# Kernel tuning notes

Hardware: AMD Instinct MI355X
Metric: run time of the kernel (lower is better)

Reference implementation:

```python
import jax, jax.numpy as jnp
import numpy as np

B, NV, NC, K = 2048, 1000, 4260, 3      # formulas, vars, clauses, literals/clause
NODES = 2 * NV + NC + 1                  # per-sample: pos lits | neg lits | clauses | root
N = B * NODES
C = B * NC


def setup_inputs() -> dict:
    key = jax.random.key(0)
    k1, k2 = jax.random.split(key)
    base = jnp.arange(B, dtype=jnp.int32) * NODES
    # positive / negative literal node ids (neg literal i is nv positions after pos literal i)
    pos_idx = (base[:, None] + jnp.arange(NV, dtype=jnp.int32)).ravel()
    neg_idx = pos_idx + NV
    # each clause picks K random literals from its own sample's 2*NV literal nodes
    lits = jax.random.randint(k1, (B, NC, K), 0, 2 * NV, dtype=jnp.int32)
    or_src = (lits + base[:, None, None]).ravel()              # [E] literal node per OR edge
    or_seg = jnp.repeat(jnp.arange(C, dtype=jnp.int32), K)     # [E] clause id per OR edge
    and_seg = jnp.repeat(jnp.arange(B, dtype=jnp.int32), NC)   # [C] root id per clause
    emb = jax.random.uniform(k2, (N,), dtype=jnp.float32)      # soft assignments in [0,1]
    return {"emb": emb, "pos_idx": pos_idx, "neg_idx": neg_idx,
            "or_src": or_src, "or_seg": or_seg, "and_seg": and_seg,
            "n_clauses": C, "n_roots": B, "epoch": 10}


def reference(emb, pos_idx, neg_idx, or_src, or_seg, and_seg, n_clauses, n_roots, epoch):
    t = jnp.asarray(epoch, jnp.float32) ** (-1.2)  # annealing temperature
    # literal transform: temporary[ind==1] = 1 - emb[ind==0]
    lit = emb.at[neg_idx].set(1.0 - emb[pos_idx])
    # --- OR gates: temperature-scaled soft-max over each clause's literals ---
    v = lit[or_src]                                            # [E] gathered literal values
    m = jax.ops.segment_max(v, or_seg, num_segments=n_clauses)
    w = jnp.exp((v - m[or_seg]) / t)                           # stabilized exp weights
    num = jax.ops.segment_sum(v * w, or_seg, num_segments=n_clauses)
    den = jax.ops.segment_sum(w, or_seg, num_segments=n_clauses)
    clause = num / den                                         # [C] soft-OR per clause
    # --- AND gate: temperature-scaled soft-min over each sample's clauses ---
    mn = jax.ops.segment_min(clause, and_seg, num_segments=n_roots)
    w2 = jnp.exp(-(clause - mn[and_seg]) / t)
    num2 = jax.ops.segment_sum(clause * w2, and_seg, num_segments=n_roots)
    den2 = jax.ops.segment_sum(w2, and_seg, num_segments=n_roots)
    return num2 / den2                                         # [B] soft-SAT per sample
```

## Files before the change

kernel.cpp:

```cpp
#include <hip/hip_runtime.h>

#define TPB 256


__device__ __forceinline__ float softor3(float a, float b, float c, float invt) {
    float m  = fmaxf(fmaxf(a, b), c);
    float wa = __expf((a - m) * invt);
    float wb = __expf((b - m) * invt);
    float wc = __expf((c - m) * invt);
    return fmaf(a, wa, fmaf(b, wb, c * wc)) / (wa + wb + wc);
}

__global__ __launch_bounds__(TPB, 8) void soft_sat_kernel(
    const float* __restrict__ emb,
    const int*   __restrict__ or_src,
    const int*   __restrict__ epoch_p,
    float* __restrict__ out,
    int NV, int NC, int NODES)
{
    extern __shared__ float smem[];
    float* lit = smem;
    float* red = smem + 2 * NV;

    const int b     = blockIdx.x;
    const int tid   = threadIdx.x;
    const int lane  = tid & 63;
    const int wid   = tid >> 6;
    const int baseI = b * NODES;

    const float invt = powf((float)epoch_p[0], 1.2f);

    const float* embb = emb + baseI;
    for (int i = tid; i < NV; i += TPB) {
        float e = embb[i];
        lit[i]      = e;
        lit[i + NV] = 1.0f - e;
    }
    __syncthreads();

    const int* osb = or_src + (long long)b * NC * 3;

    float mn = 3.4e38f, n2 = 0.0f, d2 = 0.0f;

    int c0 = 0;
    for (; c0 + TPB * 4 <= NC; c0 += TPB * 4) {
        const int4* p = (const int4*)(osb + (c0 + tid * 4) * 3);
        int4 A = p[0], Bv = p[1], Cv = p[2];

        float cv0 = softor3(lit[A.x  - baseI], lit[A.y  - baseI], lit[A.z  - baseI], invt);
        float cv1 = softor3(lit[A.w  - baseI], lit[Bv.x - baseI], lit[Bv.y - baseI], invt);
        float cv2 = softor3(lit[Bv.z - baseI], lit[Bv.w - baseI], lit[Cv.x - baseI], invt);
        float cv3 = softor3(lit[Cv.y - baseI], lit[Cv.z - baseI], lit[Cv.w - baseI], invt);

        float cmin = fminf(fminf(cv0, cv1), fminf(cv2, cv3));
        float m = fminf(mn, cmin);
        float f = __expf((m - mn) * invt);
        n2 *= f; d2 *= f; mn = m;

        float w0 = __expf((mn - cv0) * invt);
        float w1 = __expf((mn - cv1) * invt);
        float w2 = __expf((mn - cv2) * invt);
        float w3 = __expf((mn - cv3) * invt);
        n2 = fmaf(cv0, w0, fmaf(cv1, w1, fmaf(cv2, w2, fmaf(cv3, w3, n2))));
        d2 += w0 + w1 + w2 + w3;
    }

    for (int c = c0 + tid; c < NC; c += TPB) {
        const int* q = osb + c * 3;
        float cv = softor3(lit[q[0] - baseI], lit[q[1] - baseI], lit[q[2] - baseI], invt);
        float m = fminf(mn, cv);
        float f = __expf((m - mn) * invt);
        n2 *= f; d2 *= f; mn = m;
        float w = __expf((mn - cv) * invt);
        n2 = fmaf(cv, w, n2);
        d2 += w;
    }

    for (int off = 32; off; off >>= 1) {
        float mo = __shfl_xor(mn, off);
        float no = __shfl_xor(n2, off);
        float dd = __shfl_xor(d2, off);
        float m  = fminf(mn, mo);
        float f1 = __expf((m - mn) * invt);
        float f2 = __expf((m - mo) * invt);
        n2 = n2 * f1 + no * f2;
        d2 = d2 * f1 + dd * f2;
        mn = m;
    }
    if (lane == 0) { red[wid * 3] = mn; red[wid * 3 + 1] = n2; red[wid * 3 + 2] = d2; }
    __syncthreads();

    if (tid == 0) {
        float M = red[0], N2 = red[1], D2 = red[2];
        for (int w = 1; w < TPB / 64; ++w) {
            float mo = red[w * 3], no = red[w * 3 + 1], dd = red[w * 3 + 2];
            float m  = fminf(M, mo);
            float f1 = __expf((m - M) * invt);
            float f2 = __expf((m - mo) * invt);
            N2 = N2 * f1 + no * f2;
            D2 = D2 * f1 + dd * f2;
            M = m;
        }
        out[b] = N2 / D2;
    }
}

extern "C" void kernel_launch(void* const* d_in, const int* in_sizes, int n_in,
                              void* d_out, int out_size, void* d_ws, size_t ws_size,
                              hipStream_t stream)
{
    const float* emb     = (const float*)d_in[0];
    const int*   or_src  = (const int*)d_in[3];
    const int*   epoch_p = (const int*)d_in[8];
    float*       out     = (float*)d_out;

    const int B     = out_size;
    const int NV    = in_sizes[1] / B;
    const int NODES = in_sizes[0] / B;
    const int C     = in_sizes[5];
    const int NC    = C / B;

    const size_t smem = (size_t)(2 * NV + 12) * sizeof(float);
    soft_sat_kernel<<<B, TPB, smem, stream>>>(emb, or_src, epoch_p, out,
                                              NV, NC, NODES);
}
```

Before: 250.2 us.

## Prefetch clause indices ahead of LDS fill and double-buffer 8 clauses per thread

Loads each thread's clause literal indices before the shared-memory literal fill, and software-pipelines the next chunk's index loads while the current chunk is being evaluated. Each thread now handles 8 clauses per iteration instead of 4. Launch bounds are relaxed to 4 blocks per SM to make room for the extra registers. The goal is to hide global-load latency on the index stream, at the cost of higher register pressure and possibly lower occupancy.

Result: no change. 251.5 us (+0.5%).

```diff
diff --git a/kernel.cpp b/kernel.cpp
--- a/kernel.cpp
+++ b/kernel.cpp
@@ -11,7 +11,9 @@
     return fmaf(a, wa, fmaf(b, wb, c * wc)) / (wa + wb + wc);
 }
 
-__global__ __launch_bounds__(TPB, 8) void soft_sat_kernel(
+#define CL(v0, v1, v2) softor3(lit[(v0) - baseI], lit[(v1) - baseI], lit[(v2) - baseI], invt)
+
+__global__ __launch_bounds__(TPB, 4) void soft_sat_kernel(
     const float* __restrict__ emb,
     const int*   __restrict__ or_src,
     const int*   __restrict__ epoch_p,
@@ -30,6 +32,15 @@
 
     const float invt = powf((float)epoch_p[0], 1.2f);
 
+    const int* osb  = or_src + (long long)b * NC * 3;
+    const int nfull = (NC / (TPB * 8)) * (TPB * 8);
+
+    int4 a0, a1, a2, a3, a4, a5;
+    if (nfull) {
+        const int4* p = (const int4*)(osb + tid * 24);
+        a0 = p[0]; a1 = p[1]; a2 = p[2]; a3 = p[3]; a4 = p[4]; a5 = p[5];
+    }
+
     const float* embb = emb + baseI;
     for (int i = tid; i < NV; i += TPB) {
         float e = embb[i];
@@ -38,21 +49,27 @@
     }
     __syncthreads();
 
-    const int* osb = or_src + (long long)b * NC * 3;
-
     float mn = 3.4e38f, n2 = 0.0f, d2 = 0.0f;
 
-    int c0 = 0;
-    for (; c0 + TPB * 4 <= NC; c0 += TPB * 4) {
-        const int4* p = (const int4*)(osb + (c0 + tid * 4) * 3);
-        int4 A = p[0], Bv = p[1], Cv = p[2];
+    for (int c0 = 0; c0 < nfull; c0 += TPB * 8) {
+        int4 b0, b1, b2, b3, b4, b5;
+        const int cn = c0 + TPB * 8;
+        if (cn < nfull) {
+            const int4* p = (const int4*)(osb + (cn + tid * 8) * 3);
+            b0 = p[0]; b1 = p[1]; b2 = p[2]; b3 = p[3]; b4 = p[4]; b5 = p[5];
+        }
 
-        float cv0 = softor3(lit[A.x  - baseI], lit[A.y  - baseI], lit[A.z  - baseI], invt);
-        float cv1 = softor3(lit[A.w  - baseI], lit[Bv.x - baseI], lit[Bv.y - baseI], invt);
-        float cv2 = softor3(lit[Bv.z - baseI], lit[Bv.w - baseI], lit[Cv.x - baseI], invt);
-        float cv3 = softor3(lit[Cv.y - baseI], lit[Cv.z - baseI], lit[Cv.w - baseI], invt);
+        float cv0 = CL(a0.x, a0.y, a0.z);
+        float cv1 = CL(a0.w, a1.x, a1.y);
+        float cv2 = CL(a1.z, a1.w, a2.x);
+        float cv3 = CL(a2.y, a2.z, a2.w);
+        float cv4 = CL(a3.x, a3.y, a3.z);
+        float cv5 = CL(a3.w, a4.x, a4.y);
+        float cv6 = CL(a4.z, a4.w, a5.x);
+        float cv7 = CL(a5.y, a5.z, a5.w);
 
-        float cmin = fminf(fminf(cv0, cv1), fminf(cv2, cv3));
+        float cmin = fminf(fminf(fminf(cv0, cv1), fminf(cv2, cv3)),
+                           fminf(fminf(cv4, cv5), fminf(cv6, cv7)));
         float m = fminf(mn, cmin);
         float f = __expf((m - mn) * invt);
         n2 *= f; d2 *= f; mn = m;
@@ -61,13 +78,20 @@
         float w1 = __expf((mn - cv1) * invt);
         float w2 = __expf((mn - cv2) * invt);
         float w3 = __expf((mn - cv3) * invt);
+        float w4 = __expf((mn - cv4) * invt);
+        float w5 = __expf((mn - cv5) * invt);
+        float w6 = __expf((mn - cv6) * invt);
+        float w7 = __expf((mn - cv7) * invt);
         n2 = fmaf(cv0, w0, fmaf(cv1, w1, fmaf(cv2, w2, fmaf(cv3, w3, n2))));
-        d2 += w0 + w1 + w2 + w3;
+        n2 = fmaf(cv4, w4, fmaf(cv5, w5, fmaf(cv6, w6, fmaf(cv7, w7, n2))));
+        d2 += (w0 + w1 + w2 + w3) + (w4 + w5 + w6 + w7);
+
+        if (cn < nfull) { a0 = b0; a1 = b1; a2 = b2; a3 = b3; a4 = b4; a5 = b5; }
     }
 
-    for (int c = c0 + tid; c < NC; c += TPB) {
+    for (int c = nfull + tid; c < NC; c += TPB) {
         const int* q = osb + c * 3;
-        float cv = softor3(lit[q[0] - baseI], lit[q[1] - baseI], lit[q[2] - baseI], invt);
+        float cv = CL(q[0], q[1], q[2]);
         float m = fminf(mn, cv);
         float f = __expf((m - mn) * invt);
         n2 *= f; d2 *= f; mn = m;
```
